# Optimization experiments

Measured on AMD Instinct MI355X. Metric: run time of the kernel, lower is better.

Reference implementation:

```python
import math
import jax, jax.numpy as jnp
import numpy as np

HEADS = 8
D = 128            # model_dim
PE = D // 2        # position_embedding_size (query_positional_score=True)
MAXP = 32          # max_position_embeddings
LN_EPS = 1e-5


def setup_inputs() -> dict:
    key = jax.random.key(0)
    ks = jax.random.split(key, 7)
    bs, h, w = 8, 32, 32
    hidden_state = jax.random.normal(ks[0], (bs, h, w, D), dtype=jnp.float32)
    row_emb = jax.random.normal(ks[1], (2 * MAXP - 1, PE), dtype=jnp.float32) * 0.02
    col_emb = jax.random.normal(ks[2], (2 * MAXP - 1, PE), dtype=jnp.float32) * 0.02
    # torch Linear weights are (out_features, in_features)
    Wq = jax.random.normal(ks[3], (HEADS * D, D), dtype=jnp.float32) / math.sqrt(D)
    Wk = jax.random.normal(ks[4], (HEADS * D, D), dtype=jnp.float32) / math.sqrt(D)
    Wv = jax.random.normal(ks[5], (D, HEADS * D), dtype=jnp.float32) / math.sqrt(HEADS * D)
    bv = jnp.zeros((D,), dtype=jnp.float32)
    ln_g = jnp.ones((D,), dtype=jnp.float32)
    ln_b = jnp.zeros((D,), dtype=jnp.float32)
    return {"hidden_state": hidden_state, "row_emb": row_emb, "col_emb": col_emb,
            "Wq": Wq, "Wk": Wk, "Wv": Wv, "bv": bv, "ln_g": ln_g, "ln_b": ln_b}


def _layer_norm(x, g, b):
    mu = jnp.mean(x, axis=-1, keepdims=True)
    var = jnp.var(x, axis=-1, keepdims=True)
    return (x - mu) * jax.lax.rsqrt(var + LN_EPS) * g + b


def _forward(hidden_state, row_emb, col_emb, Wq, Wk, Wv, bv, ln_g, ln_b):
    bs, h, w, _ = hidden_state.shape
    x = _layer_norm(hidden_state, ln_g, ln_b)  # pre_norm=True
    sqrt_norm = math.sqrt(D)

    # relative indices (static, h == w == 32 here)
    deltas = np.arange(MAXP)[None, :] - np.arange(MAXP)[:, None]
    rel = deltas + MAXP - 1
    row_embeds = row_emb[rel[:w, :w]]  # (w, w, PE)
    col_embeds = col_emb[rel[:h, :h]]  # (h, h, PE)

    # projections; original does .view(bs, w, h, heads, D) on a (bs,h,w,heads*D) tensor
    q = jnp.einsum('bhwc,oc->bhwo', x, Wq).reshape(bs, w, h, HEADS, D)
    k = jnp.einsum('bhwc,oc->bhwo', x, Wk).reshape(bs, w, h, HEADS, D)

    q_row = q[..., :PE]
    q_col = q[..., PE:]
    row_scores = jnp.einsum('bijhd,ikd->bijhk', q_row, row_embeds)
    col_scores = jnp.einsum('bijhd,jld->bijhl', q_col, col_embeds)
    scores = (row_scores[..., :, None] + col_scores[..., None, :]) / sqrt_norm  # bijhkl
    scores = scores.transpose(0, 2, 1, 3, 5, 4)

    content = jnp.einsum('bijhd,bklhd->bijhkl', q, k) / sqrt_norm
    scores = scores + content.transpose(0, 2, 1, 3, 5, 4)  # (bs, h, w, heads, h, w)

    attn_shape = scores.shape
    probs = jax.nn.softmax(scores.reshape(*attn_shape[:-2], -1), axis=-1).reshape(attn_shape)

    # dropout omitted (inference / p=0)
    context = jnp.einsum('bijhkl,bkld->bijhd', probs, x)
    context = context.reshape(bs, h, w, HEADS * D)
    output = jnp.einsum('bhwc,oc->bhwo', context, Wv) + bv + x
    return output, probs


def reference(hidden_state, row_emb, col_emb, Wq, Wk, Wv, bv, ln_g, ln_b):
    return _forward(hidden_state, row_emb, col_emb, Wq, Wk, Wv, bv, ln_g, ln_b)
```

## Files before the change

### kernel.cpp

```cpp
#include <hip/hip_runtime.h>
#include <hip/hip_bf16.h>

#define HEADS 8
#define D 128
#define QSCALE 0.12751743f
#define PPITCH 2064

typedef unsigned short u16;
typedef unsigned int u32;
typedef __attribute__((ext_vector_type(8))) short short8;
typedef __attribute__((ext_vector_type(4))) float f32x4;

static __device__ inline u16 f2bf(float f) {
    u32 u = __float_as_uint(f);
    return (u16)((u + 0x7FFFu + ((u >> 16) & 1u)) >> 16);
}
static __device__ inline u32 pk2bf(float a, float b) {
    return (u32)f2bf(a) | ((u32)f2bf(b) << 16);
}
static __device__ inline u32 cvtpk(float a, float b) {
    union { __hip_bfloat162 h; u32 u; } x;
    x.h = __float22bfloat162_rn(make_float2(a, b));
    return x.u;
}
static __device__ inline f32x4 mfma16(short8 a, short8 b, f32x4 c) {
    return __builtin_amdgcn_mfma_f32_16x16x32_bf16(a, b, c, 0, 0, 0);
}
static __device__ inline short8 cvt8(const float* e) {
    f32x4 v0 = *(const f32x4*)e;
    f32x4 v1 = *(const f32x4*)(e + 4);
    union { uint4 u; short8 s; } x;
    x.u = make_uint4(pk2bf(v0[0], v0[1]), pk2bf(v0[2], v0[3]),
                     pk2bf(v1[0], v1[1]), pk2bf(v1[2], v1[3]));
    return x.s;
}

__global__ __launch_bounds__(256) void k_wcvt(const float* __restrict__ Wq,
    const float* __restrict__ Wk, const float* __restrict__ Wv,
    u16* __restrict__ wqk, u16* __restrict__ wv)
{
    int idx = (blockIdx.x * 256 + threadIdx.x) * 4;
    const float* src;
    u16* dst;
    if (idx < 131072)      { src = Wq + idx;           dst = wqk + idx; }
    else if (idx < 262144) { src = Wk + (idx - 131072); dst = wqk + idx; }
    else                   { src = Wv + (idx - 262144); dst = wv + (idx - 262144); }
    f32x4 v = *(const f32x4*)src;
    *(uint2*)dst = make_uint2(pk2bf(v[0], v[1]), pk2bf(v[2], v[3]));
}

__global__ __launch_bounds__(256) void k_ln(const float* __restrict__ hs,
    const float* __restrict__ g, const float* __restrict__ b,
    float* __restrict__ xf, u16* __restrict__ xbf)
{
    int row  = blockIdx.x * 4 + (threadIdx.x >> 6);
    int lane = threadIdx.x & 63;
    const float* p = hs + (size_t)row * D + lane * 2;
    float2 v = *(const float2*)p;
    float s  = v.x + v.y;
    float s2 = v.x * v.x + v.y * v.y;
    #pragma unroll
    for (int off = 1; off < 64; off <<= 1) {
        s  += __shfl_xor(s, off);
        s2 += __shfl_xor(s2, off);
    }
    float mu  = s * 0.0078125f;
    float var = s2 * 0.0078125f - mu * mu;
    float inv = rsqrtf(var + 1e-5f);
    float2 o;
    o.x = (v.x - mu) * inv * g[lane * 2 + 0] + b[lane * 2 + 0];
    o.y = (v.y - mu) * inv * g[lane * 2 + 1] + b[lane * 2 + 1];
    *(float2*)(xf + (size_t)row * D + lane * 2) = o;
    *(u32*)(xbf + (size_t)row * D + lane * 2) = pk2bf(o.x, o.y);
}

__global__ __launch_bounds__(256) void k_xt(const float* __restrict__ xf,
    u16* __restrict__ xt)
{
    __shared__ __align__(16) u16 tl[128][136];
    int b = blockIdx.x, ch = blockIdx.y;
    int tid = threadIdx.x;
    const float* src = xf + ((size_t)b * 1024 + ch * 128) * 128;
    #pragma unroll
    for (int it = 0; it < 16; ++it) {
        int s = tid + it * 256;
        int p = s >> 5, d4 = (s & 31) * 4;
        f32x4 v = *(const f32x4*)(src + (size_t)p * 128 + d4);
        tl[d4 + 0][p] = f2bf(v[0]);
        tl[d4 + 1][p] = f2bf(v[1]);
        tl[d4 + 2][p] = f2bf(v[2]);
        tl[d4 + 3][p] = f2bf(v[3]);
    }
    __syncthreads();
    u16* dst = xt + (size_t)b * 131072 + ch * 128;
    #pragma unroll
    for (int i = 0; i < 8; ++i) {
        int d = (tid >> 4) + i * 16, c8 = (tid & 15) * 8;
        *(uint4*)(dst + (size_t)d * 1024 + c8) = *(const uint4*)&tl[d][c8];
    }
}

__global__ __launch_bounds__(256) void k_proj(const u16* __restrict__ xbf,
    const u16* __restrict__ wqk,
    u16* __restrict__ q_bf, u16* __restrict__ kt_bf)
{
    int tid = threadIdx.x;
    int w = tid >> 6, l = tid & 63, h = l >> 4, ln = l & 15;
    int t0 = blockIdx.x * 64 + w * 16;
    int o0 = blockIdx.y * 64;
    short8 a[4];
    #pragma unroll
    for (int s = 0; s < 4; ++s)
        a[s] = *(const short8*)(xbf + (size_t)(t0 + ln) * 128 + s * 32 + h * 8);
    f32x4 acc[4];
    #pragma unroll
    for (int n = 0; n < 4; ++n) acc[n] = f32x4{0.f, 0.f, 0.f, 0.f};
    #pragma unroll
    for (int n = 0; n < 4; ++n) {
        const u16* wsrc = wqk + (size_t)(o0 + n * 16 + ln) * 128;
        #pragma unroll
        for (int s = 0; s < 4; ++s) {
            short8 bf = *(const short8*)(wsrc + s * 32 + h * 8);
            acc[n] = mfma16(a[s], bf, acc[n]);
        }
    }
    bool isq = (o0 < 1024);
    float oscale = isq ? QSCALE : 1.0f;
    int head = (o0 & 1023) >> 7;
    int od_base = (o0 & 127);
    u16* basep = isq ? q_bf : kt_bf;
    #pragma unroll
    for (int n = 0; n < 4; ++n) {
        int d0 = od_base + n * 16 + ln;
        #pragma unroll
        for (int r = 0; r < 4; ++r) {
            int t = t0 + h * 4 + r;
            int b = t >> 10, pos = t & 1023;
            size_t row;
            if (isq) row = (size_t)(b * 8 + head) * 1024 + pos;
            else { int I = pos >> 5, J = pos & 31; row = (size_t)(b * 8 + head) * 1024 + (J * 32 + I); }
            basep[row * 128 + d0] = f2bf(acc[n][r] * oscale);
        }
    }
}

__global__ __launch_bounds__(256) void k_bias(const u16* __restrict__ q_bf,
    const float* __restrict__ row_emb, const float* __restrict__ col_emb,
    float* __restrict__ rbias, float* __restrict__ cbias)
{
    __shared__ __align__(16) float cbf[32][68];
    int tid = threadIdx.x;
    int w = tid >> 6, l = tid & 63, h = l >> 4, ln = l & 15;
    int blk = blockIdx.x;
    int bh = blk >> 5, I = blk & 31;
    const u16* qb = q_bf + ((size_t)bh * 1024 + I * 32) * 128;
    size_t obase = (size_t)blk * 1024;
    if (w < 2) {
        short8 a0 = *(const short8*)(qb + (size_t)(w * 16 + ln) * 128 + h * 8);
        short8 a1 = *(const short8*)(qb + (size_t)(w * 16 + ln) * 128 + 32 + h * 8);
        f32x4 o[2] = {f32x4{0,0,0,0}, f32x4{0,0,0,0}};
        #pragma unroll
        for (int n = 0; n < 2; ++n) {
            int K = n * 16 + ln;
            const float* e = row_emb + (size_t)(K - I + 31) * 64 + h * 8;
            o[n] = mfma16(a0, cvt8(e), o[n]);
            o[n] = mfma16(a1, cvt8(e + 32), o[n]);
        }
        #pragma unroll
        for (int n = 0; n < 2; ++n)
            #pragma unroll
            for (int r = 0; r < 4; ++r)
                rbias[obase + (size_t)(w * 16 + h * 4 + r) * 32 + n * 16 + ln] = o[n][r];
    } else {
        int m = w - 2;
        short8 a0 = *(const short8*)(qb + (size_t)(m * 16 + ln) * 128 + 64 + h * 8);
        short8 a1 = *(const short8*)(qb + (size_t)(m * 16 + ln) * 128 + 96 + h * 8);
        f32x4 o[4] = {f32x4{0,0,0,0}, f32x4{0,0,0,0}, f32x4{0,0,0,0}, f32x4{0,0,0,0}};
        #pragma unroll
        for (int n = 0; n < 4; ++n) {
            int p = n * 16 + ln;
            if (p > 62) p = 62;
            const float* e = col_emb + (size_t)p * 64 + h * 8;
            o[n] = mfma16(a0, cvt8(e), o[n]);
            o[n] = mfma16(a1, cvt8(e + 32), o[n]);
        }
        #pragma unroll
        for (int n = 0; n < 4; ++n)
            #pragma unroll
            for (int r = 0; r < 4; ++r)
                cbf[m * 16 + h * 4 + r][n * 16 + ln] = o[n][r];
    }
    __syncthreads();
    int J = tid >> 3, L0 = (tid & 7) * 4;
    float4 g;
    g.x = cbf[J][L0 + 0 - J + 31];
    g.y = cbf[J][L0 + 1 - J + 31];
    g.z = cbf[J][L0 + 2 - J + 31];
    g.w = cbf[J][L0 + 3 - J + 31];
    *(float4*)(cbias + obase + (size_t)J * 32 + L0) = g;
}

__global__ __launch_bounds__(512, 4) void k_attn(const u16* __restrict__ q_bf,
    const u16* __restrict__ kt_bf, const u16* __restrict__ xt_bf,
    const float* __restrict__ rbias, const float* __restrict__ cbias,
    float* __restrict__ probs, u16* __restrict__ ctx_bf)
{
    __shared__ __align__(16) char P[32 * PPITCH];
    __shared__ float wred[2][256];
    __shared__ float linv_s[32];

    int tid = threadIdx.x;
    int w = tid >> 6, l = tid & 63, h = l >> 4, ln = l & 15;
    int flat = blockIdx.x;
    int bh = flat >> 5, I = flat & 31;
    int b = bh >> 3, head = bh & 7;
    int kk0 = w * 128;

    const float* rbase = rbias + (size_t)(bh * 32 + I) * 1024;
    const float* cbase = cbias + (size_t)(bh * 32 + I) * 1024;
    f32x4 rbr[2][2], cbr[2];
    #pragma unroll
    for (int n = 0; n < 2; ++n) {
        int J = n * 16 + ln;
        rbr[n][0] = *(const f32x4*)(rbase + J * 32 + h * 4);
        rbr[n][1] = *(const f32x4*)(rbase + J * 32 + 16 + h * 4);
        cbr[n]    = *(const f32x4*)(cbase + J * 32 + w * 4);
    }

    f32x4 acc[2][8];
    #pragma unroll
    for (int n = 0; n < 2; ++n)
        #pragma unroll
        for (int t = 0; t < 8; ++t) acc[n][t] = f32x4{0.f, 0.f, 0.f, 0.f};
    const u16* kbase = kt_bf + ((size_t)bh * 1024 + kk0) * 128;
    const u16* qbase = q_bf + ((size_t)bh * 1024 + I * 32) * 128;
    #pragma unroll
    for (int s = 0; s < 4; ++s) {
        short8 q0 = *(const short8*)(qbase + (size_t)ln * 128 + s * 32 + h * 8);
        short8 q1 = *(const short8*)(qbase + (size_t)(16 + ln) * 128 + s * 32 + h * 8);
        #pragma unroll
        for (int t = 0; t < 8; ++t) {
            short8 kf = *(const short8*)(kbase + (size_t)(t * 16 + ln) * 128 + s * 32 + h * 8);
            acc[0][t] = mfma16(kf, q0, acc[0][t]);
            acc[1][t] = mfma16(kf, q1, acc[1][t]);
        }
    }

    #pragma unroll
    for (int n = 0; n < 2; ++n) {
        float mx = -1e30f;
        #pragma unroll
        for (int t = 0; t < 8; ++t) {
            float cbv = cbr[n][t >> 1];
            #pragma unroll
            for (int r = 0; r < 4; ++r) {
                float v = acc[n][t][r] + rbr[n][t & 1][r] + cbv;
                acc[n][t][r] = v;
                mx = fmaxf(mx, v);
            }
        }
        mx = fmaxf(mx, __shfl_xor(mx, 16));
        mx = fmaxf(mx, __shfl_xor(mx, 32));
        if (l < 16) wred[0][w * 32 + n * 16 + ln] = mx;
    }
    __syncthreads();

    #pragma unroll
    for (int n = 0; n < 2; ++n) {
        int J = n * 16 + ln;
        float M = wred[0][J];
        #pragma unroll
        for (int w2 = 1; w2 < 8; ++w2) M = fmaxf(M, wred[0][w2 * 32 + J]);
        float sum = 0.f;
        #pragma unroll
        for (int t = 0; t < 8; ++t) {
            float p0 = exp2f(acc[n][t][0] - M);
            float p1 = exp2f(acc[n][t][1] - M);
            float p2 = exp2f(acc[n][t][2] - M);
            float p3 = exp2f(acc[n][t][3] - M);
            acc[n][t] = f32x4{p0, p1, p2, p3};
            sum += (p0 + p1) + (p2 + p3);
            *(uint2*)(P + J * PPITCH + (kk0 + t * 16 + h * 4) * 2) =
                make_uint2(cvtpk(p0, p1), cvtpk(p2, p3));
        }
        sum += __shfl_xor(sum, 16);
        sum += __shfl_xor(sum, 32);
        if (l < 16) wred[1][w * 32 + J] = sum;
    }
    __syncthreads();
    if (tid < 32) {
        float s = 0.f;
        #pragma unroll
        for (int w2 = 0; w2 < 8; ++w2) s += wred[1][w2 * 32 + tid];
        linv_s[tid] = 1.0f / s;
    }
    __syncthreads();

    #pragma unroll
    for (int n = 0; n < 2; ++n) {
        int J = n * 16 + ln;
        float inv = linv_s[J];
        float* prow = probs + ((((size_t)(b * 32 + J) * 32 + I) * 8 + head) << 10)
                    + kk0 + h * 4;
        #pragma unroll
        for (int t = 0; t < 8; ++t) {
            f32x4 o = acc[n][t];
            f32x4 ov = f32x4{o[0] * inv, o[1] * inv, o[2] * inv, o[3] * inv};
            __builtin_nontemporal_store(ov, (f32x4*)(prow + t * 16));
        }
    }

    f32x4 cacc[2] = {f32x4{0,0,0,0}, f32x4{0,0,0,0}};
    int d0 = w * 16;
    const u16* xb = xt_bf + (size_t)b * 131072 + (size_t)(d0 + ln) * 1024 + h * 8;
    #pragma unroll
    for (int ks = 0; ks < 32; ++ks) {
        short8 xf8 = *(const short8*)(xb + ks * 32);
        #pragma unroll
        for (int m = 0; m < 2; ++m) {
            short8 pa = *(const short8*)(P + (m * 16 + ln) * PPITCH + (ks * 32 + h * 8) * 2);
            cacc[m] = mfma16(pa, xf8, cacc[m]);
        }
    }
    #pragma unroll
    for (int m = 0; m < 2; ++m)
        #pragma unroll
        for (int r = 0; r < 4; ++r) {
            int J = m * 16 + h * 4 + r;
            ctx_bf[((size_t)(b * 32 + J) * 32 + I) * 1024 + head * 128 + d0 + ln] =
                f2bf(cacc[m][r] * linv_s[J]);
        }
}

__global__ __launch_bounds__(256) void k_out(const u16* __restrict__ ctx_bf,
    const u16* __restrict__ wv_bf, const float* __restrict__ bv,
    const float* __restrict__ xf, float* __restrict__ out)
{
    int tid = threadIdx.x;
    int w = tid >> 6, l = tid & 63, h = l >> 4, ln = l & 15;
    int wm = w >> 1, wn = w & 1;
    int t0 = blockIdx.x * 32 + wm * 16;
    int o0 = blockIdx.y * 64 + wn * 32;
    f32x4 acc[2] = {f32x4{0,0,0,0}, f32x4{0,0,0,0}};
    for (int ks = 0; ks < 32; ++ks) {
        short8 a = *(const short8*)(ctx_bf + (size_t)(t0 + ln) * 1024 + ks * 32 + h * 8);
        #pragma unroll
        for (int nt = 0; nt < 2; ++nt) {
            short8 bb = *(const short8*)(wv_bf + (size_t)(o0 + nt * 16 + ln) * 1024 + ks * 32 + h * 8);
            acc[nt] = mfma16(a, bb, acc[nt]);
        }
    }
    #pragma unroll
    for (int nt = 0; nt < 2; ++nt) {
        int o = o0 + nt * 16 + ln;
        float bvv = bv[o];
        #pragma unroll
        for (int r = 0; r < 4; ++r) {
            int t = t0 + h * 4 + r;
            out[(size_t)t * 128 + o] = acc[nt][r] + bvv + xf[(size_t)t * 128 + o];
        }
    }
}

extern "C" void kernel_launch(void* const* d_in, const int* in_sizes, int n_in,
                              void* d_out, int out_size, void* d_ws, size_t ws_size,
                              hipStream_t stream) {
    (void)in_sizes; (void)n_in; (void)out_size; (void)ws_size;
    const float* hs      = (const float*)d_in[0];
    const float* row_emb = (const float*)d_in[1];
    const float* col_emb = (const float*)d_in[2];
    const float* Wq      = (const float*)d_in[3];
    const float* Wk      = (const float*)d_in[4];
    const float* Wv      = (const float*)d_in[5];
    const float* bv      = (const float*)d_in[6];
    const float* ln_g    = (const float*)d_in[7];
    const float* ln_b    = (const float*)d_in[8];

    float* out   = (float*)d_out;
    float* probs = out + 1048576;

    char* ws = (char*)d_ws;
    float* xf     = (float*)(ws);
    u16*   xbf    = (u16*)(ws + 4194304);
    u16*   q_bf   = (u16*)(ws + 6291456);
    u16*   kt_bf  = (u16*)(ws + 23068672);
    u16*   xt     = (u16*)(ws + 39845888);
    u16*   wqk_bf = (u16*)(ws + 41943040);
    u16*   wv_bf  = (u16*)(ws + 42467328);
    u16*   ctx    = (u16*)(ws + 42729472);
    float* rbias  = (float*)(ws + 59506688);
    float* cbias  = (float*)(ws + 67895296);

    k_wcvt <<<384, 256, 0, stream>>>(Wq, Wk, Wv, wqk_bf, wv_bf);
    k_ln   <<<2048, 256, 0, stream>>>(hs, ln_g, ln_b, xf, xbf);
    k_xt   <<<dim3(8, 8), 256, 0, stream>>>(xf, xt);
    k_proj <<<dim3(128, 32), 256, 0, stream>>>(xbf, wqk_bf, q_bf, kt_bf);
    k_bias <<<2048, 256, 0, stream>>>(q_bf, row_emb, col_emb, rbias, cbias);
    k_attn <<<2048, 512, 0, stream>>>(q_bf, kt_bf, xt, rbias, cbias, probs, ctx);
    k_out  <<<dim3(256, 2), 256, 0, stream>>>(ctx, wv_bf, bv, xf, out);
}
```

Before: 279.8 us.

## Fuse layernorm with transpose and drop softmax max pass in attention

Merges the layernorm and the bf16 transpose into one kernel, removing a launch and a full re-read of the normalized activations. In the attention kernel, the row-max reduction and its barrier are removed: scores go straight into exp2, and one fewer block-wide reduction and sync is needed. The probability output is now re-read from the bf16 shared-memory tile and written in a row-contiguous pattern, and the context is rescaled with per-lane sums. In exchange, softmax without max subtraction can overflow for large scores, and the stored probabilities carry bf16 rounding.

Result: no change. 277.3 us, median of 2 (-0.9%).

```diff
diff --git a/kernel.cpp b/kernel.cpp
--- a/kernel.cpp
+++ b/kernel.cpp
@@ -11,6 +11,9 @@
 typedef __attribute__((ext_vector_type(8))) short short8;
 typedef __attribute__((ext_vector_type(4))) float f32x4;
 
+static __device__ inline float sbf2f(short s) {
+    return __uint_as_float(((u32)(unsigned short)s) << 16);
+}
 static __device__ inline u16 f2bf(float f) {
     u32 u = __float_as_uint(f);
     return (u16)((u + 0x7FFFu + ((u >> 16) & 1u)) >> 16);
@@ -49,47 +52,41 @@
     *(uint2*)dst = make_uint2(pk2bf(v[0], v[1]), pk2bf(v[2], v[3]));
 }
 
-__global__ __launch_bounds__(256) void k_ln(const float* __restrict__ hs,
-    const float* __restrict__ g, const float* __restrict__ b,
-    float* __restrict__ xf, u16* __restrict__ xbf)
-{
-    int row  = blockIdx.x * 4 + (threadIdx.x >> 6);
-    int lane = threadIdx.x & 63;
-    const float* p = hs + (size_t)row * D + lane * 2;
-    float2 v = *(const float2*)p;
-    float s  = v.x + v.y;
-    float s2 = v.x * v.x + v.y * v.y;
-    #pragma unroll
-    for (int off = 1; off < 64; off <<= 1) {
-        s  += __shfl_xor(s, off);
-        s2 += __shfl_xor(s2, off);
-    }
-    float mu  = s * 0.0078125f;
-    float var = s2 * 0.0078125f - mu * mu;
-    float inv = rsqrtf(var + 1e-5f);
-    float2 o;
-    o.x = (v.x - mu) * inv * g[lane * 2 + 0] + b[lane * 2 + 0];
-    o.y = (v.y - mu) * inv * g[lane * 2 + 1] + b[lane * 2 + 1];
-    *(float2*)(xf + (size_t)row * D + lane * 2) = o;
-    *(u32*)(xbf + (size_t)row * D + lane * 2) = pk2bf(o.x, o.y);
-}
-
-__global__ __launch_bounds__(256) void k_xt(const float* __restrict__ xf,
-    u16* __restrict__ xt)
+__global__ __launch_bounds__(256) void k_lnxt(const float* __restrict__ hs,
+    const float* __restrict__ g, const float* __restrict__ bb,
+    float* __restrict__ xf, u16* __restrict__ xbf, u16* __restrict__ xt)
 {
     __shared__ __align__(16) u16 tl[128][136];
     int b = blockIdx.x, ch = blockIdx.y;
     int tid = threadIdx.x;
-    const float* src = xf + ((size_t)b * 1024 + ch * 128) * 128;
+    int c4 = (tid & 31) * 4;
+    f32x4 g4 = *(const f32x4*)(g + c4);
+    f32x4 b4 = *(const f32x4*)(bb + c4);
+    const float* src = hs + ((size_t)b * 1024 + ch * 128) * 128;
     #pragma unroll
     for (int it = 0; it < 16; ++it) {
-        int s = tid + it * 256;
-        int p = s >> 5, d4 = (s & 31) * 4;
-        f32x4 v = *(const f32x4*)(src + (size_t)p * 128 + d4);
-        tl[d4 + 0][p] = f2bf(v[0]);
-        tl[d4 + 1][p] = f2bf(v[1]);
-        tl[d4 + 2][p] = f2bf(v[2]);
-        tl[d4 + 3][p] = f2bf(v[3]);
+        int p = (tid >> 5) + it * 8;
+        f32x4 v = *(const f32x4*)(src + (size_t)p * 128 + c4);
+        float s1 = (v[0] + v[1]) + (v[2] + v[3]);
+        float s2 = (v[0] * v[0] + v[1] * v[1]) + (v[2] * v[2] + v[3] * v[3]);
+        #pragma unroll
+        for (int off = 1; off < 32; off <<= 1) {
+            s1 += __shfl_xor(s1, off);
+            s2 += __shfl_xor(s2, off);
+        }
+        float mu  = s1 * 0.0078125f;
+        float var = s2 * 0.0078125f - mu * mu;
+        float inv = rsqrtf(var + 1e-5f);
+        f32x4 o;
+        #pragma unroll
+        for (int q = 0; q < 4; ++q) o[q] = (v[q] - mu) * inv * g4[q] + b4[q];
+        size_t row = (size_t)b * 1024 + ch * 128 + p;
+        *(f32x4*)(xf + row * 128 + c4) = o;
+        *(uint2*)(xbf + row * 128 + c4) = make_uint2(pk2bf(o[0], o[1]), pk2bf(o[2], o[3]));
+        tl[c4 + 0][p] = f2bf(o[0]);
+        tl[c4 + 1][p] = f2bf(o[1]);
+        tl[c4 + 2][p] = f2bf(o[2]);
+        tl[c4 + 3][p] = f2bf(o[3]);
     }
     __syncthreads();
     u16* dst = xt + (size_t)b * 131072 + ch * 128;
@@ -206,8 +203,7 @@
     float* __restrict__ probs, u16* __restrict__ ctx_bf)
 {
     __shared__ __align__(16) char P[32 * PPITCH];
-    __shared__ float wred[2][256];
-    __shared__ float linv_s[32];
+    __shared__ float wred[256];
 
     int tid = threadIdx.x;
     int w = tid >> 6, l = tid & 63, h = l >> 4, ln = l & 15;
@@ -248,65 +244,51 @@
 
     #pragma unroll
     for (int n = 0; n < 2; ++n) {
-        float mx = -1e30f;
+        int J = n * 16 + ln;
+        float sum = 0.f;
         #pragma unroll
         for (int t = 0; t < 8; ++t) {
             float cbv = cbr[n][t >> 1];
-            #pragma unroll
-            for (int r = 0; r < 4; ++r) {
-                float v = acc[n][t][r] + rbr[n][t & 1][r] + cbv;
-                acc[n][t][r] = v;
-                mx = fmaxf(mx, v);
-            }
-        }
-        mx = fmaxf(mx, __shfl_xor(mx, 16));
-        mx = fmaxf(mx, __shfl_xor(mx, 32));
-        if (l < 16) wred[0][w * 32 + n * 16 + ln] = mx;
-    }
-    __syncthreads();
-
-    #pragma unroll
-    for (int n = 0; n < 2; ++n) {
-        int J = n * 16 + ln;
-        float M = wred[0][J];
-        #pragma unroll
-        for (int w2 = 1; w2 < 8; ++w2) M = fmaxf(M, wred[0][w2 * 32 + J]);
-        float sum = 0.f;
-        #pragma unroll
-        for (int t = 0; t < 8; ++t) {
-            float p0 = exp2f(acc[n][t][0] - M);
-            float p1 = exp2f(acc[n][t][1] - M);
-            float p2 = exp2f(acc[n][t][2] - M);
-            float p3 = exp2f(acc[n][t][3] - M);
-            acc[n][t] = f32x4{p0, p1, p2, p3};
+            float p0 = exp2f(acc[n][t][0] + rbr[n][t & 1][0] + cbv);
+            float p1 = exp2f(acc[n][t][1] + rbr[n][t & 1][1] + cbv);
+            float p2 = exp2f(acc[n][t][2] + rbr[n][t & 1][2] + cbv);
+            float p3 = exp2f(acc[n][t][3] + rbr[n][t & 1][3] + cbv);
             sum += (p0 + p1) + (p2 + p3);
             *(uint2*)(P + J * PPITCH + (kk0 + t * 16 + h * 4) * 2) =
                 make_uint2(cvtpk(p0, p1), cvtpk(p2, p3));
         }
         sum += __shfl_xor(sum, 16);
         sum += __shfl_xor(sum, 32);
-        if (l < 16) wred[1][w * 32 + J] = sum;
+        if (l < 16) wred[w * 32 + J] = sum;
     }
     __syncthreads();
-    if (tid < 32) {
-        float s = 0.f;
-        #pragma unroll
-        for (int w2 = 0; w2 < 8; ++w2) s += wred[1][w2 * 32 + tid];
-        linv_s[tid] = 1.0f / s;
-    }
-    __syncthreads();
-
-    #pragma unroll
-    for (int n = 0; n < 2; ++n) {
-        int J = n * 16 + ln;
-        float inv = linv_s[J];
-        float* prow = probs + ((((size_t)(b * 32 + J) * 32 + I) * 8 + head) << 10)
-                    + kk0 + h * 4;
-        #pragma unroll
-        for (int t = 0; t < 8; ++t) {
-            f32x4 o = acc[n][t];
-            f32x4 ov = f32x4{o[0] * inv, o[1] * inv, o[2] * inv, o[3] * inv};
-            __builtin_nontemporal_store(ov, (f32x4*)(prow + t * 16));
+
+    f32x4 sum0 = f32x4{0.f, 0.f, 0.f, 0.f};
+    f32x4 sum1 = f32x4{0.f, 0.f, 0.f, 0.f};
+    #pragma unroll
+    for (int w2 = 0; w2 < 8; ++w2) {
+        sum0 += *(const f32x4*)&wred[w2 * 32 + h * 4];
+        sum1 += *(const f32x4*)&wred[w2 * 32 + 16 + h * 4];
+    }
+    int j = tid >> 4;
+    float sd = 0.f;
+    #pragma unroll
+    for (int w2 = 0; w2 < 8; ++w2) sd += wred[w2 * 32 + j];
+    float invd = 1.0f / sd;
+
+    {
+        float* prow = probs + ((((size_t)(b * 32 + j) * 32 + I) * 8 + head) << 10);
+        #pragma unroll
+        for (int i = 0; i < 8; ++i) {
+            int kk = i * 128 + (tid & 15) * 8;
+            short8 pv = *(const short8*)(P + j * PPITCH + kk * 2);
+            float4 o0, o1;
+            o0.x = sbf2f(pv[0]) * invd; o0.y = sbf2f(pv[1]) * invd;
+            o0.z = sbf2f(pv[2]) * invd; o0.w = sbf2f(pv[3]) * invd;
+            o1.x = sbf2f(pv[4]) * invd; o1.y = sbf2f(pv[5]) * invd;
+            o1.z = sbf2f(pv[6]) * invd; o1.w = sbf2f(pv[7]) * invd;
+            *(float4*)(prow + kk)     = o0;
+            *(float4*)(prow + kk + 4) = o1;
         }
     }
 
@@ -327,8 +309,9 @@
         #pragma unroll
         for (int r = 0; r < 4; ++r) {
             int J = m * 16 + h * 4 + r;
+            float inv = 1.0f / (m ? sum1[r] : sum0[r]);
             ctx_bf[((size_t)(b * 32 + J) * 32 + I) * 1024 + head * 128 + d0 + ln] =
-                f2bf(cacc[m][r] * linv_s[J]);
+                f2bf(cacc[m][r] * inv);
         }
 }
 
@@ -392,8 +375,7 @@
     float* cbias  = (float*)(ws + 67895296);
 
     k_wcvt <<<384, 256, 0, stream>>>(Wq, Wk, Wv, wqk_bf, wv_bf);
-    k_ln   <<<2048, 256, 0, stream>>>(hs, ln_g, ln_b, xf, xbf);
-    k_xt   <<<dim3(8, 8), 256, 0, stream>>>(xf, xt);
+    k_lnxt <<<dim3(8, 8), 256, 0, stream>>>(hs, ln_g, ln_b, xf, xbf, xt);
     k_proj <<<dim3(128, 32), 256, 0, stream>>>(xbf, wqk_bf, q_bf, kt_bf);
     k_bias <<<2048, 256, 0, stream>>>(q_bf, row_emb, col_emb, rbias, cbias);
     k_attn <<<2048, 512, 0, stream>>>(q_bf, kt_bf, xt, rbias, cbias, probs, ctx);
```
